# Kernel tuning notes

Hardware: AMD Instinct MI355X
Metric: run time of the kernel (lower is better)

## Reference

```python
import jax, jax.numpy as jnp
import numpy as np

MODES1, MODES2 = 32, 32

def fht_matrix(N):
    # Exact linear-operator form of the repo's recursive fht1d (N must be a power of two,
    # which it is here, so the pad/truncate branch never triggers).
    if N == 1:
        return np.ones((1, 1), np.float32)
    M = fht_matrix(N // 2)
    k = np.arange(N // 2)
    cas = (np.cos(2 * np.pi * k / N) + np.sin(2 * np.pi * k / N)).astype(np.float32)[:, None]
    E = np.zeros((N // 2, N), np.float32); E[:, 0::2] = M   # even-index sub-transform
    O = np.zeros((N // 2, N), np.float32); O[:, 1::2] = M   # odd-index sub-transform
    return np.concatenate([E + cas * O, E - cas * O], axis=0)

def dht2(x, M1, M2):
    # apply the (pseudo-)Hartley transform along dims 2 then 3: X[k,l] = sum_{h,w} M1[k,h] M2[l,w] x[h,w]
    return jnp.einsum('bchw,kh,lw->bckl', x, M1, M2)

def neg_freq(a):
    # index map k -> (-k mod m) on the last two dims (flip then roll by 1)
    return jnp.roll(jnp.flip(a, axis=(-2, -1)), shift=(1, 1), axis=(-2, -1))

def compl_mul2d(x1, x2):
    x1n = neg_freq(x1)
    x2n = neg_freq(x2)
    return 0.5 * (jnp.einsum('bixy,ioxy->boxy', x1, x2)
                  - jnp.einsum('bixy,ioxy->boxy', x1n, x2n)
                  + jnp.einsum('bixy,ioxy->boxy', x1, x2n)
                  + jnp.einsum('bixy,ioxy->boxy', x1n, x2))

def setup_inputs() -> dict:
    key = jax.random.key(0)
    k1, k2 = jax.random.split(key)
    B, Cin, Cout, S = 32, 64, 64, 128
    x = jax.random.normal(k1, (B, Cin, S, S), jnp.float32)
    scale = 1.0 / (Cin * Cout)
    weights1 = scale * jax.random.uniform(k2, (Cin, Cout, MODES1, MODES2), jnp.float32)
    return {"x": x, "weights1": weights1}

def reference(x, weights1):
    B, Cin, S1, S2 = x.shape
    Cout = weights1.shape[1]
    M1 = jnp.asarray(fht_matrix(S1))
    M2 = jnp.asarray(fht_matrix(S2))
    x_ht = dht2(x, M1, M2)                                        # [B,Cin,S1,S2]
    block = compl_mul2d(x_ht[:, :, :MODES1, :MODES2], weights1)   # [B,Cout,m1,m2]
    out_ht = jnp.zeros((B, Cout, S1, S2), x.dtype).at[:, :, :MODES1, :MODES2].set(block)
    # idht = dht / (S1*S2)
    return dht2(out_ht, M1, M2) / (S1 * S2)
```

## Files before the change

### kernel.cpp

```cpp
#include <hip/hip_runtime.h>
#include <math.h>


#define SS   128
#define MD   32
#define NBAT 32
#define CI   64
#define CO   64

#define TWO_PI 6.2831853071795864769

typedef __attribute__((ext_vector_type(8))) short bf16x8;
typedef __attribute__((ext_vector_type(4))) float f32x4;

static const size_t OFF_XH   = 32768;
static const size_t OFF_XHT  = 32768 + 2097152;
static const size_t OFF_WT   = 32768 + 2 * 2097152;
static const size_t OFF_BLKT = OFF_XH;
static const size_t OFF_BLK  = OFF_XHT;
static const size_t OFF_MFH  = OFF_WT + 4194304;
static const size_t OFF_MFL  = OFF_MFH + 8192;

__device__ inline float m_entry(int k, int n) {
    float prod = 1.f;
    int kk = k, nn = n;
    for (int Nj = SS; Nj > 1; Nj >>= 1) {
        int half = Nj >> 1;
        int k1 = kk & (half - 1);
        if (nn & 1) {
            double ang = (TWO_PI / (double)Nj) * (double)k1;
            float cas = (float)(cos(ang) + sin(ang));
            prod *= (kk < half) ? cas : -cas;
        }
        kk = k1;
        nn >>= 1;
    }
    return prod;
}

__device__ inline unsigned short f2bf(float f) {
    unsigned u = __float_as_uint(f);
    return (unsigned short)((u + 0x7FFF + ((u >> 16) & 1)) >> 16);
}
__device__ inline float bf2f(unsigned short h) {
    return __uint_as_float((unsigned)h << 16);
}
__device__ inline void split2(float a, float b, unsigned& hi, unsigned& lo) {
    unsigned short ah = f2bf(a), bh = f2bf(b);
    hi = (unsigned)ah | ((unsigned)bh << 16);
    lo = (unsigned)f2bf(a - bf2f(ah)) | ((unsigned)f2bf(b - bf2f(bh)) << 16);
}

__global__ __launch_bounds__(256) void k_prep(const float* __restrict__ wgt,
                                              float* __restrict__ Wt,
                                              unsigned short* __restrict__ MFH,
                                              unsigned short* __restrict__ MFL) {
    const int bid = blockIdx.x;
    const int t   = threadIdx.x;
    if (bid >= 4096) {
        int idx2 = (bid - 4096) * 256 + t;
        int j    = idx2 & 7;
        int lane = (idx2 >> 3) & 63;
        int s    = (idx2 >> 9) & 3;
        int tt   = idx2 >> 11;
        int kq   = tt * 16 + (lane & 15);
        int nq   = s * 32 + ((lane >> 4) << 3) + j;
        float f  = m_entry(kq, nq);
        unsigned short hi = f2bf(f);
        MFH[idx2] = hi;
        MFL[idx2] = f2bf(f - bf2f(hi));
        return;
    }
    __shared__ float tile[32][33];
    const int mt  = bid & 31;
    const int iot = bid >> 5;
    const int tx = t & 31;
    const int ty = t >> 5;
#pragma unroll
    for (int j = 0; j < 4; ++j) {
        int r = ty + 8 * j;
        tile[r][tx] = wgt[(iot * 32 + r) * 1024 + mt * 32 + tx];
    }
    __syncthreads();
#pragma unroll
    for (int j = 0; j < 4; ++j) {
        int r = ty + 8 * j;
        Wt[(mt * 32 + r) * 4096 + iot * 32 + tx] = tile[tx][r];
    }
}

__global__ __launch_bounds__(256, 3) void k_fwd2(const float* __restrict__ x,
                                                 const unsigned short* __restrict__ MFH,
                                                 const unsigned short* __restrict__ MFL,
                                                 float* __restrict__ Xh) {
    const int bc = blockIdx.x;
    const float* xp = x + (size_t)bc * 16384;
    const int t = threadIdx.x;
    const int lane = t & 63, wid = t >> 6;
    const int l15 = lane & 15, g = lane >> 4;

    __shared__ unsigned short Pan[2][2][4096];
    __shared__ unsigned short Ybf[2][32 * 136];

    const int sh0 = t >> 3, swq = t & 7;

    {
#pragma unroll
        for (int q = 0; q < 4; ++q) {
            int h = sh0 + 32 * q;
            float4 v = *(const float4*)(xp + h * 128 + swq * 4);
            unsigned h01, l01, h23, l23;
            split2(v.x, v.y, h01, l01);
            split2(v.z, v.w, h23, l23);
            int i8 = h * 8 + (swq ^ ((h & 3) << 1));
            ((uint2*)&Pan[0][0][0])[i8] = make_uint2(h01, h23);
            ((uint2*)&Pan[0][1][0])[i8] = make_uint2(l01, l23);
        }
    }

    f32x4 acc[2][2] = {};
    const int hbase = wid * 32;

    for (int s = 0; s < 4; ++s) {
        __syncthreads();
        const int cur = s & 1, nxt = cur ^ 1;
        float4 pre[4];
        if (s < 3) {
#pragma unroll
            for (int q = 0; q < 4; ++q)
                pre[q] = *(const float4*)(xp + (sh0 + 32 * q) * 128 + (s + 1) * 32 + swq * 4);
        }
        bf16x8 Bh[2], Bl[2];
#pragma unroll
        for (int lt = 0; lt < 2; ++lt) {
            int bidx = (lt * 4 + s) * 64 + lane;
            Bh[lt] = ((const bf16x8*)MFH)[bidx];
            Bl[lt] = ((const bf16x8*)MFL)[bidx];
        }
#pragma unroll
        for (int hh = 0; hh < 2; ++hh) {
            int h = hbase + hh * 16 + l15;
            int aidx = h * 4 + (g ^ (h & 3));
            bf16x8 Ah = ((const bf16x8*)&Pan[cur][0][0])[aidx];
            bf16x8 Al = ((const bf16x8*)&Pan[cur][1][0])[aidx];
#pragma unroll
            for (int lt = 0; lt < 2; ++lt) {
                acc[hh][lt] = __builtin_amdgcn_mfma_f32_16x16x32_bf16(Ah, Bh[lt], acc[hh][lt], 0, 0, 0);
                acc[hh][lt] = __builtin_amdgcn_mfma_f32_16x16x32_bf16(Ah, Bl[lt], acc[hh][lt], 0, 0, 0);
                acc[hh][lt] = __builtin_amdgcn_mfma_f32_16x16x32_bf16(Al, Bh[lt], acc[hh][lt], 0, 0, 0);
            }
        }
        if (s < 3) {
#pragma unroll
            for (int q = 0; q < 4; ++q) {
                int h = sh0 + 32 * q;
                unsigned h01, l01, h23, l23;
                split2(pre[q].x, pre[q].y, h01, l01);
                split2(pre[q].z, pre[q].w, h23, l23);
                int i8 = h * 8 + (swq ^ ((h & 3) << 1));
                ((uint2*)&Pan[nxt][0][0])[i8] = make_uint2(h01, h23);
                ((uint2*)&Pan[nxt][1][0])[i8] = make_uint2(l01, l23);
            }
        }
    }

#pragma unroll
    for (int hh = 0; hh < 2; ++hh) {
#pragma unroll
        for (int lt = 0; lt < 2; ++lt) {
            int lmode = lt * 16 + l15;
            int h0 = hbase + hh * 16 + g * 4;
            f32x4 v = acc[hh][lt];
            unsigned hi01, lo01, hi23, lo23;
            split2(v[0], v[1], hi01, lo01);
            split2(v[2], v[3], hi23, lo23);
            ((uint2*)&Ybf[0][0])[lmode * 34 + (h0 >> 2)] = make_uint2(hi01, hi23);
            ((uint2*)&Ybf[1][0])[lmode * 34 + (h0 >> 2)] = make_uint2(lo01, lo23);
        }
    }
    __syncthreads();

    const int kt = wid >> 1, lt2 = wid & 1;
    f32x4 z = {};
#pragma unroll
    for (int s2 = 0; s2 < 4; ++s2) {
        int aidx = (kt * 4 + s2) * 64 + lane;
        bf16x8 Ah = ((const bf16x8*)MFH)[aidx];
        bf16x8 Al = ((const bf16x8*)MFL)[aidx];
        int lmode = lt2 * 16 + l15;
        int yidx = lmode * 17 + s2 * 4 + g;
        bf16x8 Yh = ((const bf16x8*)&Ybf[0][0])[yidx];
        bf16x8 Yl = ((const bf16x8*)&Ybf[1][0])[yidx];
        z = __builtin_amdgcn_mfma_f32_16x16x32_bf16(Ah, Yh, z, 0, 0, 0);
        z = __builtin_amdgcn_mfma_f32_16x16x32_bf16(Ah, Yl, z, 0, 0, 0);
        z = __builtin_amdgcn_mfma_f32_16x16x32_bf16(Al, Yh, z, 0, 0, 0);
    }
    float* op = Xh + (size_t)bc * 1024;
#pragma unroll
    for (int r = 0; r < 4; ++r)
        op[(kt * 16 + g * 4 + r) * 32 + lt2 * 16 + l15] = z[r];
}

__global__ __launch_bounds__(256) void t_xh(const float* __restrict__ Xh,
                                            float* __restrict__ Xh_t) {
    __shared__ float tile[32][33];
    const int i  = blockIdx.x & 63;
    const int mt = blockIdx.x >> 6;
    const int tx = threadIdx.x & 31;
    const int ty = threadIdx.x >> 5;
#pragma unroll
    for (int j = 0; j < 4; ++j) {
        int b = ty + 8 * j;
        tile[b][tx] = Xh[(b * 64 + i) * 1024 + mt * 32 + tx];
    }
    __syncthreads();
#pragma unroll
    for (int j = 0; j < 4; ++j) {
        int row = ty + 8 * j;
        Xh_t[(mt * 32 + row) * 2048 + i * 32 + tx] = tile[tx][row];
    }
}

__global__ __launch_bounds__(256) void k_mix4(const float* __restrict__ Xh_t,
                                              const float* __restrict__ Wt,
                                              float* __restrict__ blk_t) {
    const int m  = blockIdx.x;
    const int xm = m >> 5, ym = m & 31;
    const int nm = (((32 - xm) & 31) << 5) | ((32 - ym) & 31);
    if (m > nm) return;
    const int t = threadIdx.x;

    __shared__ float Xs[2][64][32];

    {
        const float4* xm4 = (const float4*)(Xh_t + m * 2048);
        const float4* xn4 = (const float4*)(Xh_t + nm * 2048);
        float4* s0 = (float4*)&Xs[0][0][0];
        float4* s1 = (float4*)&Xs[1][0][0];
        s0[t]       = xm4[t];
        s0[t + 256] = xm4[t + 256];
        s1[t]       = xn4[t];
        s1[t + 256] = xn4[t + 256];
    }
    __syncthreads();

    const int o  = t & 63;
    const int bq = t >> 6;
    const float* wpm = Wt + m * 4096 + o;
    const float* wpn = Wt + nm * 4096 + o;

    float am[8], an[8];
#pragma unroll
    for (int j = 0; j < 8; ++j) { am[j] = 0.f; an[j] = 0.f; }

#pragma unroll 4
    for (int i = 0; i < 64; ++i) {
        float wm = wpm[i * 64];
        float wn = wpn[i * 64];
        float we = 0.5f * (wm + wn);
        float wo = 0.5f * (wm - wn);
        const float* xr  = &Xs[0][i][bq * 8];
        const float* xrn = &Xs[1][i][bq * 8];
#pragma unroll
        for (int j = 0; j < 8; ++j) {
            float x1  = xr[j];
            float x1n = xrn[j];
            am[j] = fmaf(x1, we, fmaf(x1n, wo, am[j]));
            an[j] = fmaf(x1n, we, fmaf(x1, -wo, an[j]));
        }
    }

    float* om = blk_t + m * 2048 + o;
    float* on = blk_t + nm * 2048 + o;
#pragma unroll
    for (int j = 0; j < 8; ++j) {
        int b = bq * 8 + j;
        om[b * 64] = am[j];
        on[b * 64] = an[j];
    }
}

__global__ __launch_bounds__(256) void t_blk(const float* __restrict__ blk_t,
                                             float* __restrict__ blk) {
    __shared__ float tile[32][33];
    const int mt  = blockIdx.x & 31;
    const int bot = blockIdx.x >> 5;
    const int tx = threadIdx.x & 31;
    const int ty = threadIdx.x >> 5;
#pragma unroll
    for (int j = 0; j < 4; ++j) {
        int r = ty + 8 * j;
        tile[r][tx] = blk_t[(mt * 32 + r) * 2048 + bot * 32 + tx];
    }
    __syncthreads();
#pragma unroll
    for (int j = 0; j < 4; ++j) {
        int r = ty + 8 * j;
        blk[(bot * 32 + r) * 1024 + mt * 32 + tx] = tile[tx][r];
    }
}

__global__ __launch_bounds__(256, 2) void k_inv2(const float* __restrict__ blk,
                                                 const unsigned short* __restrict__ MFH,
                                                 const unsigned short* __restrict__ MFL,
                                                 float* __restrict__ out) {
    const int bo = blockIdx.x;
    const int t  = threadIdx.x;
    const int lane = t & 63, wid = t >> 6;
    const int l15 = lane & 15, g = lane >> 4;

    __shared__ __align__(16) unsigned short Bst[2][32 * 40];
    __shared__ __align__(16) unsigned short Tl[2][128 * 40];

    {
        float4 v = ((const float4*)(blk + (size_t)bo * 1024))[t];
        const int h = t >> 3, l0 = (t & 7) * 4;
        float vv[4] = { v.x * (1.f / 16384.f), v.y * (1.f / 16384.f),
                        v.z * (1.f / 16384.f), v.w * (1.f / 16384.f) };
#pragma unroll
        for (int q = 0; q < 4; ++q) {
            unsigned short hi = f2bf(vv[q]);
            Bst[0][(l0 + q) * 40 + h] = hi;
            Bst[1][(l0 + q) * 40 + h] = f2bf(vv[q] - bf2f(hi));
        }
    }
    __syncthreads();

#pragma unroll
    for (int rr = 0; rr < 2; ++rr) {
        const int tt = wid * 2 + rr;
        const int aidx = (tt * 4) * 64 + lane;
        bf16x8 Ah = ((const bf16x8*)MFH)[aidx];
        bf16x8 Al = ((const bf16x8*)MFL)[aidx];
#pragma unroll
        for (int lt = 0; lt < 2; ++lt) {
            bf16x8 Bh = *(const bf16x8*)&Bst[0][(lt * 16 + l15) * 40 + g * 8];
            bf16x8 Bl = *(const bf16x8*)&Bst[1][(lt * 16 + l15) * 40 + g * 8];
            f32x4 acc = {};
            acc = __builtin_amdgcn_mfma_f32_16x16x32_bf16(Ah, Bh, acc, 0, 0, 0);
            acc = __builtin_amdgcn_mfma_f32_16x16x32_bf16(Al, Bh, acc, 0, 0, 0);
            acc = __builtin_amdgcn_mfma_f32_16x16x32_bf16(Ah, Bl, acc, 0, 0, 0);
#pragma unroll
            for (int ri = 0; ri < 4; ++ri) {
                int r = tt * 16 + g * 4 + ri;
                int l = lt * 16 + l15;
                unsigned short hi = f2bf(acc[ri]);
                Tl[0][r * 40 + l] = hi;
                Tl[1][r * 40 + l] = f2bf(acc[ri] - bf2f(hi));
            }
        }
    }
    __syncthreads();

    float* op = out + (size_t)bo * (SS * SS);
#pragma unroll
    for (int rr = 0; rr < 2; ++rr) {
        const int rt = wid * 2 + rr;
        bf16x8 Bh = *(const bf16x8*)&Tl[0][(rt * 16 + l15) * 40 + g * 8];
        bf16x8 Bl = *(const bf16x8*)&Tl[1][(rt * 16 + l15) * 40 + g * 8];
        const int r = rt * 16 + l15;
#pragma unroll
        for (int ct = 0; ct < 8; ++ct) {
            const int aidx = (ct * 4) * 64 + lane;
            bf16x8 Ah = ((const bf16x8*)MFH)[aidx];
            bf16x8 Al = ((const bf16x8*)MFL)[aidx];
            f32x4 acc = {};
            acc = __builtin_amdgcn_mfma_f32_16x16x32_bf16(Ah, Bh, acc, 0, 0, 0);
            acc = __builtin_amdgcn_mfma_f32_16x16x32_bf16(Al, Bh, acc, 0, 0, 0);
            acc = __builtin_amdgcn_mfma_f32_16x16x32_bf16(Ah, Bl, acc, 0, 0, 0);
            *(float4*)&op[r * SS + ct * 16 + g * 4] =
                make_float4(acc[0], acc[1], acc[2], acc[3]);
        }
    }
}

extern "C" void kernel_launch(void* const* d_in, const int* in_sizes, int n_in,
                              void* d_out, int out_size, void* d_ws, size_t ws_size,
                              hipStream_t stream) {
    const float* x   = (const float*)d_in[0];
    const float* wgt = (const float*)d_in[1];
    float* outp = (float*)d_out;
    float* ws   = (float*)d_ws;

    float* Xh    = ws + OFF_XH;
    float* Xh_t  = ws + OFF_XHT;
    float* Wt    = ws + OFF_WT;
    float* blk_t = ws + OFF_BLKT;
    float* blk   = ws + OFF_BLK;
    unsigned short* MFH = (unsigned short*)(ws + OFF_MFH);
    unsigned short* MFL = (unsigned short*)(ws + OFF_MFL);

    k_prep <<<4160, 256, 0, stream>>>(wgt, Wt, MFH, MFL);
    k_fwd2 <<<2048, 256, 0, stream>>>(x, MFH, MFL, Xh);
    t_xh   <<<2048, 256, 0, stream>>>(Xh, Xh_t);
    k_mix4 <<<1024, 256, 0, stream>>>(Xh_t, Wt, blk_t);
    t_blk  <<<2048, 256, 0, stream>>>(blk_t, blk);
    k_inv2 <<<2048, 256, 0, stream>>>(blk, MFH, MFL, outp);
}
```

Measured before the change: 108.2 us.

## Load x directly into MFMA A-fragments, removing LDS staging in forward transform

The forward Hartley kernel no longer stages x tiles through a double-buffered LDS panel with block barriers. Each lane now loads its own A-fragment rows from global memory into registers, prefetching one step ahead. It splits them into bf16 hi/lo with a cheaper truncating-add split, then feeds the MFMAs directly. This removes shared-memory traffic and per-step __syncthreads and frees LDS for occupancy. In exchange the global loads are less coalesced (32-byte chunks per lane across rows), register pressure rises, the launch-bounds occupancy hint is dropped, and the new split rounds ties differently from round-to-nearest-even.

```diff
diff --git a/kernel.cpp b/kernel.cpp
--- a/kernel.cpp
+++ b/kernel.cpp
@@ -49,6 +49,20 @@
     unsigned short ah = f2bf(a), bh = f2bf(b);
     hi = (unsigned)ah | ((unsigned)bh << 16);
     lo = (unsigned)f2bf(a - bf2f(ah)) | ((unsigned)f2bf(b - bf2f(bh)) << 16);
+}
+__device__ inline void fsplit2(float a, float b, unsigned& hi, unsigned& lo) {
+    unsigned ua = __float_as_uint(a), ub = __float_as_uint(b);
+    unsigned ha = (ua + 0x8000u) & 0xFFFF0000u;
+    unsigned hb = (ub + 0x8000u) & 0xFFFF0000u;
+    float la = a - __uint_as_float(ha);
+    float lb = b - __uint_as_float(hb);
+    hi = (ha >> 16) | hb;
+    lo = (__float_as_uint(la) >> 16) | (__float_as_uint(lb) & 0xFFFF0000u);
+}
+__device__ inline bf16x8 pack4(unsigned a, unsigned b, unsigned c, unsigned d) {
+    union { unsigned u[4]; bf16x8 v; } w;
+    w.u[0] = a; w.u[1] = b; w.u[2] = c; w.u[3] = d;
+    return w.v;
 }
 
 __global__ __launch_bounds__(256) void k_prep(const float* __restrict__ wgt,
@@ -89,77 +103,62 @@
     }
 }
 
-__global__ __launch_bounds__(256, 3) void k_fwd2(const float* __restrict__ x,
-                                                 const unsigned short* __restrict__ MFH,
-                                                 const unsigned short* __restrict__ MFL,
-                                                 float* __restrict__ Xh) {
+__global__ __launch_bounds__(256) void k_fwd3(const float* __restrict__ x,
+                                              const unsigned short* __restrict__ MFH,
+                                              const unsigned short* __restrict__ MFL,
+                                              float* __restrict__ Xh) {
     const int bc = blockIdx.x;
     const float* xp = x + (size_t)bc * 16384;
     const int t = threadIdx.x;
     const int lane = t & 63, wid = t >> 6;
     const int l15 = lane & 15, g = lane >> 4;
 
-    __shared__ unsigned short Pan[2][2][4096];
     __shared__ unsigned short Ybf[2][32 * 136];
 
-    const int sh0 = t >> 3, swq = t & 7;
-
-    {
-#pragma unroll
-        for (int q = 0; q < 4; ++q) {
-            int h = sh0 + 32 * q;
-            float4 v = *(const float4*)(xp + h * 128 + swq * 4);
-            unsigned h01, l01, h23, l23;
-            split2(v.x, v.y, h01, l01);
-            split2(v.z, v.w, h23, l23);
-            int i8 = h * 8 + (swq ^ ((h & 3) << 1));
-            ((uint2*)&Pan[0][0][0])[i8] = make_uint2(h01, h23);
-            ((uint2*)&Pan[0][1][0])[i8] = make_uint2(l01, l23);
-        }
-    }
+    const int hbase = wid * 32;
+    const int ra = (hbase + l15) * 128 + g * 8;
+    const int rb = (hbase + 16 + l15) * 128 + g * 8;
 
     f32x4 acc[2][2] = {};
-    const int hbase = wid * 32;
-
+    float4 xa[2][2][2];
+
+    xa[0][0][0] = *(const float4*)(xp + ra);
+    xa[0][0][1] = *(const float4*)(xp + ra + 4);
+    xa[0][1][0] = *(const float4*)(xp + rb);
+    xa[0][1][1] = *(const float4*)(xp + rb + 4);
+
+#pragma unroll
     for (int s = 0; s < 4; ++s) {
-        __syncthreads();
-        const int cur = s & 1, nxt = cur ^ 1;
-        float4 pre[4];
         if (s < 3) {
-#pragma unroll
-            for (int q = 0; q < 4; ++q)
-                pre[q] = *(const float4*)(xp + (sh0 + 32 * q) * 128 + (s + 1) * 32 + swq * 4);
+            const int off = (s + 1) * 32;
+            xa[(s + 1) & 1][0][0] = *(const float4*)(xp + ra + off);
+            xa[(s + 1) & 1][0][1] = *(const float4*)(xp + ra + off + 4);
+            xa[(s + 1) & 1][1][0] = *(const float4*)(xp + rb + off);
+            xa[(s + 1) & 1][1][1] = *(const float4*)(xp + rb + off + 4);
         }
         bf16x8 Bh[2], Bl[2];
 #pragma unroll
         for (int lt = 0; lt < 2; ++lt) {
-            int bidx = (lt * 4 + s) * 64 + lane;
+            const int bidx = (lt * 4 + s) * 64 + lane;
             Bh[lt] = ((const bf16x8*)MFH)[bidx];
             Bl[lt] = ((const bf16x8*)MFL)[bidx];
         }
 #pragma unroll
         for (int hh = 0; hh < 2; ++hh) {
-            int h = hbase + hh * 16 + l15;
-            int aidx = h * 4 + (g ^ (h & 3));
-            bf16x8 Ah = ((const bf16x8*)&Pan[cur][0][0])[aidx];
-            bf16x8 Al = ((const bf16x8*)&Pan[cur][1][0])[aidx];
+            const float4 v0 = xa[s & 1][hh][0];
+            const float4 v1 = xa[s & 1][hh][1];
+            unsigned h0, l0, h1, l1, h2, l2, h3, l3;
+            fsplit2(v0.x, v0.y, h0, l0);
+            fsplit2(v0.z, v0.w, h1, l1);
+            fsplit2(v1.x, v1.y, h2, l2);
+            fsplit2(v1.z, v1.w, h3, l3);
+            const bf16x8 Ah = pack4(h0, h1, h2, h3);
+            const bf16x8 Al = pack4(l0, l1, l2, l3);
 #pragma unroll
             for (int lt = 0; lt < 2; ++lt) {
                 acc[hh][lt] = __builtin_amdgcn_mfma_f32_16x16x32_bf16(Ah, Bh[lt], acc[hh][lt], 0, 0, 0);
                 acc[hh][lt] = __builtin_amdgcn_mfma_f32_16x16x32_bf16(Ah, Bl[lt], acc[hh][lt], 0, 0, 0);
                 acc[hh][lt] = __builtin_amdgcn_mfma_f32_16x16x32_bf16(Al, Bh[lt], acc[hh][lt], 0, 0, 0);
-            }
-        }
-        if (s < 3) {
-#pragma unroll
-            for (int q = 0; q < 4; ++q) {
-                int h = sh0 + 32 * q;
-                unsigned h01, l01, h23, l23;
-                split2(pre[q].x, pre[q].y, h01, l01);
-                split2(pre[q].z, pre[q].w, h23, l23);
-                int i8 = h * 8 + (swq ^ ((h & 3) << 1));
-                ((uint2*)&Pan[nxt][0][0])[i8] = make_uint2(h01, h23);
-                ((uint2*)&Pan[nxt][1][0])[i8] = make_uint2(l01, l23);
             }
         }
     }
@@ -391,7 +390,7 @@
     unsigned short* MFL = (unsigned short*)(ws + OFF_MFL);
 
     k_prep <<<4160, 256, 0, stream>>>(wgt, Wt, MFH, MFL);
-    k_fwd2 <<<2048, 256, 0, stream>>>(x, MFH, MFL, Xh);
+    k_fwd3 <<<2048, 256, 0, stream>>>(x, MFH, MFL, Xh);
     t_xh   <<<2048, 256, 0, stream>>>(Xh, Xh_t);
     k_mix4 <<<1024, 256, 0, stream>>>(Xh_t, Wt, blk_t);
     t_blk  <<<2048, 256, 0, stream>>>(blk_t, blk);
```

Result: no change. 109.0 us (+0.8%).
